# Performance work log

Measured on AMD Instinct MI355X. Metric: run time of the kernel, lower is better.

The kernel has to match this reference:

```python
import jax, jax.numpy as jnp
import numpy as np

B, NX, W, DX, DY, D, H, P = 8, 512, 16, 1536, 1024, 768, 12, 8


def setup_inputs() -> dict:
    key = jax.random.key(0)
    ks = jax.random.split(key, 12)
    r = lambda k, s: jax.random.normal(k, s, dtype=jnp.float32) * 0.02
    return {
        "x": jax.random.normal(ks[0], (B, NX, DX), jnp.float32),
        "y": jax.random.normal(ks[1], (B, NX * W, DY), jnp.float32),
        "Wx": r(ks[2], (DX, D)), "bx": jnp.zeros((D,), jnp.float32),
        "Wy": r(ks[3], (DY, D)), "by": jnp.zeros((D,), jnp.float32),
        "prompt": r(ks[4], (1, P, D)),
        "Wq": r(ks[5], (D, D)), "bq": jnp.zeros((D,), jnp.float32),
        "Wk": r(ks[6], (D, D)), "bk": jnp.zeros((D,), jnp.float32),
        "Wv": r(ks[7], (D, D)), "bv": jnp.zeros((D,), jnp.float32),
        "Wo": r(ks[8], (D, D)), "bo": jnp.zeros((D,), jnp.float32),
        "ln_g": jnp.ones((D,), jnp.float32), "ln_b": jnp.zeros((D,), jnp.float32),
    }


def _l2n(f, eps=1e-6):
    return f / (jnp.linalg.norm(f, axis=-1, keepdims=True) + eps)


def reference(x, y, Wx, bx, Wy, by, prompt, Wq, bq, Wk, bk, Wv, bv, Wo, bo, ln_g, ln_b):
    dh = D // H
    scale = 1.0 / jnp.sqrt(jnp.float32(dh))
    xp = _l2n(x @ Wx + bx)            # [B,NX,D]
    yp = _l2n(y @ Wy + by)            # [B,NX*W,D]
    # In the original, only normalized_output[:,0:1] is kept per window, and
    # per-query attention is independent, so only query index 0 contributes.
    q = ((xp[:, 0] @ Wq) + bq).reshape(B, H, dh) * scale   # [B,H,dh]
    yw = yp.reshape(B, NX, W, D)                            # 16-token windows
    k = ((yw @ Wk) + bk).reshape(B, NX, W, H, dh)
    v = ((yw @ Wv) + bv).reshape(B, NX, W, H, dh)
    s = jnp.einsum('bhd,bnwhd->bhnw', q, k)                # [B,H,NX,W]
    a = jax.nn.softmax(s, axis=-1)
    ctx = jnp.einsum('bhnw,bnwhd->bnhd', a, v).reshape(B, NX, D)
    o = ctx @ Wo + bo                                      # attn out_proj
    mu = jnp.mean(o, axis=-1, keepdims=True)
    var = jnp.var(o, axis=-1, keepdims=True)
    normed = (o - mu) / jnp.sqrt(var + 1e-6) * ln_g + ln_b  # [B,NX,D]
    blocks = jnp.concatenate(
        [normed[:, :, None, :],
         jnp.broadcast_to(prompt[:, None], (B, NX, P, D))], axis=2)  # [B,NX,1+P,D]
    return blocks.reshape(B, NX * (1 + P), D)
```

## Files before the change

kernel.cpp:

```cpp
#include <hip/hip_runtime.h>
#include <stdint.h>

#define BQ 8
#define NXQ 512
#define WQ 16
#define DXQ 1536
#define DYQ 1024
#define DQ 768
#define HQ 12
#define PQ 8
#define MY 65536
#define BN_ROWS 4096

typedef __attribute__((ext_vector_type(8))) short short8;
typedef __attribute__((ext_vector_type(4))) float f32x4;
typedef unsigned short ushort_t;
typedef unsigned int uint_t;

__device__ __forceinline__ ushort_t f2bf(float f) {
  uint_t u = __float_as_uint(f);
  u += 0x7FFFu + ((u >> 16) & 1u);
  return (ushort_t)(u >> 16);
}
__device__ __forceinline__ float bf2f(ushort_t h) {
  return __uint_as_float(((uint_t)h) << 16);
}
__device__ __forceinline__ void gload_lds16(const void* g, void* l) {
  __builtin_amdgcn_global_load_lds(
      (__attribute__((address_space(1))) unsigned int*)(g),
      (__attribute__((address_space(3))) unsigned int*)(l), 16, 0, 0);
}

__global__ void k_conv(const float* __restrict__ y, const float* __restrict__ Wy,
                       const float* __restrict__ Wv, const float* __restrict__ Wo,
                       ushort_t* __restrict__ ybf, ushort_t* __restrict__ WyT,
                       ushort_t* __restrict__ WvT, ushort_t* __restrict__ WoT,
                       float* __restrict__ rowsq, float* __restrict__ oS12,
                       float* __restrict__ xw) {
  const int gstride = gridDim.x * blockDim.x;
  const int g0 = blockIdx.x * blockDim.x + threadIdx.x;
  const int NY8 = MY * DYQ / 8;
  for (int i = g0; i < NY8; i += gstride) {
    const float4* s = (const float4*)(y + (size_t)i * 8);
    float4 f0 = s[0], f1 = s[1];
    short8 hv;
    hv[0] = (short)f2bf(f0.x); hv[1] = (short)f2bf(f0.y);
    hv[2] = (short)f2bf(f0.z); hv[3] = (short)f2bf(f0.w);
    hv[4] = (short)f2bf(f1.x); hv[5] = (short)f2bf(f1.y);
    hv[6] = (short)f2bf(f1.z); hv[7] = (short)f2bf(f1.w);
    *(short8*)(ybf + (size_t)i * 8) = hv;
  }
  for (int i = g0; i < MY; i += gstride) rowsq[i] = 0.f;
  for (int i = g0; i < 2 * BN_ROWS; i += gstride) oS12[i] = 0.f;
  for (int i = g0; i < BQ * DQ; i += gstride) xw[i] = 0.f;
  const int N1 = DQ * DYQ;
  const int N2 = DQ * DQ;
  const int total = N1 + 2 * N2;
  for (int i = g0; i < total; i += gstride) {
    if (i < N1) {
      int n = i / DYQ, k = i - n * DYQ;
      WyT[i] = f2bf(Wy[k * DQ + n]);
    } else if (i < N1 + N2) {
      int j = i - N1;
      int n = j / DQ, k = j - n * DQ;
      WvT[j] = f2bf(Wv[k * DQ + n]);
    } else {
      int j = i - N1 - N2;
      int n = j / DQ, k = j - n * DQ;
      WoT[j] = f2bf(Wo[k * DQ + n]);
    }
  }
}

__global__ __launch_bounds__(128) void k_q1(const float* __restrict__ x,
                                            const float* __restrict__ Wx,
                                            const float* __restrict__ bx,
                                            float* __restrict__ xw) {
  const int b = blockIdx.x, c = blockIdx.y * 128 + threadIdx.x;
  const int kc = blockIdx.z;
  const float* xr = x + (size_t)b * NXQ * DXQ + kc * 192;
  const float* wp = Wx + (size_t)kc * 192 * DQ + c;
  float acc = (kc == 0) ? bx[c] : 0.f;
  for (int k = 0; k < 192; ++k) acc += xr[k] * wp[(size_t)k * DQ];
  atomicAdd(&xw[b * DQ + c], acc);
}

__global__ __launch_bounds__(128) void k_q2(const float* __restrict__ xw,
                                            const float* __restrict__ Wq,
                                            const float* __restrict__ bq,
                                            float* __restrict__ qv) {
  const int b = blockIdx.x, c = blockIdx.y * 128 + threadIdx.x;
  const float* xr = xw + b * DQ;
  float acc = 0.f, ss = 0.f;
  for (int k = 0; k < DQ; ++k) {
    float v = xr[k];
    acc += v * Wq[(size_t)k * DQ + c];
    ss += v * v;
  }
  const float inv = 1.0f / (sqrtf(ss) + 1e-6f);
  qv[b * DQ + c] = (acc * inv + bq[c]) * 0.125f;
}

__global__ void k_q3(const float* __restrict__ Wk, const float* __restrict__ bk,
                     const float* __restrict__ qv, float* __restrict__ qk,
                     float* __restrict__ cQ) {
  const int bh = blockIdx.x;
  const int b = bh / HQ, h = bh - b * HQ;
  const int tid = threadIdx.x;
  const float* q = qv + b * DQ + h * 64;
#pragma unroll
  for (int j = 0; j < 3; ++j) {
    int dd = tid + j * 256;
    float acc = 0.f;
    for (int j2 = 0; j2 < 64; ++j2) acc += Wk[(size_t)dd * DQ + h * 64 + j2] * q[j2];
    qk[(size_t)bh * DQ + dd] = acc;
  }
  if (tid == 0) {
    float acc = 0.f;
    for (int j2 = 0; j2 < 64; ++j2) acc += q[j2] * bk[h * 64 + j2];
    cQ[bh] = acc;
  }
}

__global__ __launch_bounds__(512, 1) void k_gemm_yp(const ushort_t* __restrict__ ybf,
                                                    const ushort_t* __restrict__ WyT,
                                                    const float* __restrict__ by,
                                                    ushort_t* __restrict__ z,
                                                    float* __restrict__ rowsqg) {
  __shared__ __align__(16) char smem[131072 + 1024];
  float* rowsq_l = (float*)(smem + 131072);
  const int tid = threadIdx.x, lane = tid & 63, wv = tid >> 6;
  const int wvM = wv >> 2, wvN = wv & 3;
  const int g = blockIdx.x;
  const int m = (g / 24) * 8 + (g & 7);
  const int n = (g >> 3) % 3;
  const int mBase = m * 256, nBase = n * 256;
  if (tid < 256) rowsq_l[tid] = 0.f;

  const int sr = lane >> 2;
  const int sc = (lane & 3) ^ (sr & 3);
  const ushort_t* aQ[2]; const ushort_t* bQ[2];
  int qDst[2];
#pragma unroll
  for (int j = 0; j < 2; ++j) {
    int r = wv * 32 + j * 16 + sr;
    aQ[j] = ybf + (size_t)(mBase + r) * DYQ + sc * 8;
    bQ[j] = WyT + (size_t)(nBase + r) * DYQ + sc * 8;
    qDst[j] = (wv * 32 + j * 16) * 64;
  }
  const int q = lane >> 4;
  int aFr[8], bFr[4];
#pragma unroll
  for (int mf = 0; mf < 8; ++mf) {
    int r = wvM * 128 + mf * 16 + (lane & 15);
    aFr[mf] = r * 64 + ((q ^ (r & 3)) << 4);
  }
#pragma unroll
  for (int nf = 0; nf < 4; ++nf) {
    int r = wvN * 64 + nf * 16 + (lane & 15);
    bFr[nf] = 16384 + r * 64 + ((q ^ (r & 3)) << 4);
  }

#define YP_STAGE(pp)                                                           \
  {                                                                            \
    char* db = smem + ((pp) & 3) * 32768;                                      \
    const int koff = ((pp) >> 1) * 64 + ((pp) & 1) * 32;                       \
    _Pragma("unroll") for (int j = 0; j < 2; ++j)                              \
        gload_lds16(aQ[j] + koff, db + qDst[j]);                               \
    _Pragma("unroll") for (int j = 0; j < 2; ++j)                              \
        gload_lds16(bQ[j] + koff, db + 16384 + qDst[j]);                       \
  }

  f32x4 acc[8][4] = {};
  YP_STAGE(0);
  YP_STAGE(1);
  YP_STAGE(2);
  asm volatile("s_waitcnt vmcnt(8)" ::: "memory");
  __builtin_amdgcn_s_barrier();
  __builtin_amdgcn_sched_barrier(0);

  for (int t = 0; t < 16; ++t) {
#pragma unroll
    for (int ks = 0; ks < 2; ++ks) {
      const int p = 2 * t + ks;
      const char* cb = smem + (p & 3) * 32768;
      short8 af[8], bf[4];
#pragma unroll
      for (int mf = 0; mf < 8; ++mf) af[mf] = *(const short8*)(cb + aFr[mf]);
#pragma unroll
      for (int nf = 0; nf < 4; ++nf) bf[nf] = *(const short8*)(cb + bFr[nf]);
      if (p <= 28) YP_STAGE(p + 3);
      asm volatile("s_waitcnt lgkmcnt(0)" ::: "memory");
      __builtin_amdgcn_sched_barrier(0);
      __builtin_amdgcn_s_setprio(1);
#pragma unroll
      for (int nf = 0; nf < 4; ++nf)
#pragma unroll
        for (int mf = 0; mf < 8; ++mf)
          acc[mf][nf] = __builtin_amdgcn_mfma_f32_16x16x32_bf16(af[mf], bf[nf],
                                                                acc[mf][nf], 0, 0, 0);
      __builtin_amdgcn_s_setprio(0);
      __builtin_amdgcn_sched_barrier(0);
      if (p <= 28) {
        asm volatile("s_waitcnt vmcnt(8)" ::: "memory");
      } else if (p == 29) {
        asm volatile("s_waitcnt vmcnt(4)" ::: "memory");
      } else {
        asm volatile("s_waitcnt vmcnt(0)" ::: "memory");
      }
      __builtin_amdgcn_s_barrier();
      __builtin_amdgcn_sched_barrier(0);
    }
  }
  __syncthreads();

  float byv[4];
#pragma unroll
  for (int nf = 0; nf < 4; ++nf) byv[nf] = by[nBase + wvN * 64 + nf * 16 + (lane & 15)];
#pragma unroll
  for (int mf = 0; mf < 8; ++mf) {
#pragma unroll
    for (int rr = 0; rr < 4; ++rr) {
      int row_l = wvM * 128 + mf * 16 + (lane >> 4) * 4 + rr;
      float ss = 0.f;
#pragma unroll
      for (int nf = 0; nf < 4; ++nf) {
        float zv = acc[mf][nf][rr] + byv[nf];
        ss += zv * zv;
        int col_l = wvN * 64 + nf * 16 + (lane & 15);
        *(ushort_t*)(smem + row_l * 512 + col_l * 2) = f2bf(zv);
      }
#pragma unroll
      for (int o = 1; o < 16; o <<= 1) ss += __shfl_xor(ss, o, 64);
      if ((lane & 15) == 0) atomicAdd(&rowsq_l[row_l], ss);
    }
  }
  __syncthreads();
  if (tid < 256) atomicAdd(&rowsqg[mBase + tid], rowsq_l[tid]);
#pragma unroll
  for (int it = 0; it < 16; ++it) {
    int row = it * 16 + (tid >> 5);
    int ch = tid & 31;
    uint4 v = *(const uint4*)(smem + row * 512 + ch * 16);
    *(uint4*)(z + (size_t)(mBase + row) * DQ + nBase + ch * 8) = v;
  }
}

__global__ __launch_bounds__(256) void k_attn(const ushort_t* __restrict__ z,
                                              const float* __restrict__ rowsqg,
                                              const float* __restrict__ qk,
                                              const float* __restrict__ cQ,
                                              ushort_t* __restrict__ p) {
  __shared__ __align__(16) char smem[16 * 1552 + 192 * 4 * 2 + 64];
  float* s_l = (float*)(smem + 16 * 1552);
  float* a_l = s_l + 192;
  float* inv_l = a_l + 192;
  const int bn = blockIdx.x, b = bn >> 9;
  const int tid = threadIdx.x;
  if (tid < 16) inv_l[tid] = 1.0f / (sqrtf(rowsqg[bn * 16 + tid]) + 1e-6f);
  for (int j = tid; j < 16 * 96; j += 256) {
    int w = j / 96, ch = j - w * 96;
    *(short8*)(smem + w * 1552 + ch * 16) =
        *(const short8*)(z + ((size_t)bn * 16 + w) * DQ + ch * 8);
  }
  __syncthreads();
  if (tid < 192) {
    int h = tid >> 4, w = tid & 15;
    const float4* qkp = (const float4*)(qk + (size_t)(b * HQ + h) * DQ);
    float acc = 0.f;
    const char* yrow = smem + w * 1552;
    for (int dc = 0; dc < 192; ++dc) {
      float4 q4 = qkp[dc];
      uint2 hh = *(const uint2*)(yrow + dc * 8);
      acc += q4.x * bf2f((ushort_t)(hh.x & 0xffff));
      acc += q4.y * bf2f((ushort_t)(hh.x >> 16));
      acc += q4.z * bf2f((ushort_t)(hh.y & 0xffff));
      acc += q4.w * bf2f((ushort_t)(hh.y >> 16));
    }
    s_l[tid] = acc * inv_l[w] + cQ[b * HQ + h];
  }
  __syncthreads();
  if (tid < 12) {
    float mx = -1e30f;
#pragma unroll
    for (int w = 0; w < 16; ++w) mx = fmaxf(mx, s_l[tid * 16 + w]);
    float sm = 0.f, ev[16];
#pragma unroll
    for (int w = 0; w < 16; ++w) {
      ev[w] = __expf(s_l[tid * 16 + w] - mx);
      sm += ev[w];
    }
    float rden = 1.0f / sm;
#pragma unroll
    for (int w = 0; w < 16; ++w) a_l[tid * 16 + w] = ev[w] * rden * inv_l[w];
  }
  __syncthreads();
  float zr[16][3];
#pragma unroll
  for (int w = 0; w < 16; ++w)
#pragma unroll
    for (int i = 0; i < 3; ++i)
      zr[w][i] = bf2f(*(const ushort_t*)(smem + w * 1552 + (tid + i * 256) * 2));
  for (int h = 0; h < HQ; ++h) {
    float acc0 = 0.f, acc1 = 0.f, acc2 = 0.f;
#pragma unroll
    for (int w = 0; w < 16; ++w) {
      float aw = a_l[h * 16 + w];
      acc0 += aw * zr[w][0];
      acc1 += aw * zr[w][1];
      acc2 += aw * zr[w][2];
    }
    size_t base = ((size_t)bn * HQ + h) * DQ + tid;
    p[base] = f2bf(acc0);
    p[base + 256] = f2bf(acc1);
    p[base + 512] = f2bf(acc2);
  }
}

#define PV_TSZ 24576
__global__ __launch_bounds__(256) void k_gemm_pv(const ushort_t* __restrict__ p,
                                                 const ushort_t* __restrict__ WvT,
                                                 const float* __restrict__ bv,
                                                 ushort_t* __restrict__ ctx) {
  __shared__ __align__(16) char smem[3 * PV_TSZ];
  const int tid = threadIdx.x, lane = tid & 63, wv = tid >> 6;
  const int wvM = wv >> 1, wvN = wv & 1;
  const int mBase = blockIdx.x * 128, h = blockIdx.y;
  const int l8 = lane >> 3;
  const int c8 = (lane & 7) ^ (l8 & 7);
  const ushort_t* aSrc[4]; const ushort_t* bSrc[2];
  int aDst[4], bDst[2];
#pragma unroll
  for (int j = 0; j < 4; ++j) {
    int r = wv * 32 + j * 8 + l8;
    aSrc[j] = p + ((size_t)(mBase + r) * HQ + h) * DQ + c8 * 8;
    aDst[j] = (wv * 32 + j * 8) * 128;
  }
#pragma unroll
  for (int j = 0; j < 2; ++j) {
    int r = wv * 16 + j * 8 + l8;
    bSrc[j] = WvT + (size_t)(h * 64 + r) * DQ + c8 * 8;
    bDst[j] = 16384 + (wv * 16 + j * 8) * 128;
  }
  const int q = lane >> 4;
  int aRowB[4], aSw[4], bRowB[2], bSw[2];
#pragma unroll
  for (int mf = 0; mf < 4; ++mf) {
    int r = wvM * 64 + mf * 16 + (lane & 15);
    aRowB[mf] = r * 128; aSw[mf] = r & 7;
  }
#pragma unroll
  for (int nf = 0; nf < 2; ++nf) {
    int r = wvN * 32 + nf * 16 + (lane & 15);
    bRowB[nf] = 16384 + r * 128; bSw[nf] = r & 7;
  }
#define PV_STAGE(dbuf, t)                                                      \
  {                                                                            \
    char* db = smem + (dbuf) * PV_TSZ;                                         \
    _Pragma("unroll") for (int j = 0; j < 4; ++j)                              \
        gload_lds16(aSrc[j] + (t) * 64, db + aDst[j]);                         \
    _Pragma("unroll") for (int j = 0; j < 2; ++j)                              \
        gload_lds16(bSrc[j] + (t) * 64, db + bDst[j]);                         \
  }
  f32x4 acc[4][2] = {};
  PV_STAGE(0, 0);
  PV_STAGE(1, 1);
  int bR = 0, bS = 2;
  for (int t = 0; t < 12; ++t) {
    if (t < 11) {
      asm volatile("s_waitcnt vmcnt(6)" ::: "memory");
    } else {
      asm volatile("s_waitcnt vmcnt(0)" ::: "memory");
    }
    __builtin_amdgcn_s_barrier();
    __builtin_amdgcn_sched_barrier(0);
    if (t + 2 < 12) PV_STAGE(bS, t + 2);
    const char* cur = smem + bR * PV_TSZ;
#pragma unroll
    for (int ks = 0; ks < 2; ++ks) {
      short8 af[4], bf[2];
#pragma unroll
      for (int mf = 0; mf < 4; ++mf)
        af[mf] = *(const short8*)(cur + aRowB[mf] + (((ks * 4 + q) ^ aSw[mf]) << 4));
#pragma unroll
      for (int nf = 0; nf < 2; ++nf)
        bf[nf] = *(const short8*)(cur + bRowB[nf] + (((ks * 4 + q) ^ bSw[nf]) << 4));
#pragma unroll
      for (int nf = 0; nf < 2; ++nf)
#pragma unroll
        for (int mf = 0; mf < 4; ++mf)
          acc[mf][nf] = __builtin_amdgcn_mfma_f32_16x16x32_bf16(af[mf], bf[nf],
                                                                acc[mf][nf], 0, 0, 0);
    }
    bR = (bR == 2) ? 0 : bR + 1;
    bS = (bS == 2) ? 0 : bS + 1;
  }
#pragma unroll
  for (int nf = 0; nf < 2; ++nf) {
    int col = h * 64 + wvN * 32 + nf * 16 + (lane & 15);
    float bvv = bv[col];
#pragma unroll
    for (int mf = 0; mf < 4; ++mf)
#pragma unroll
      for (int rr = 0; rr < 4; ++rr) {
        int row = mBase + wvM * 64 + mf * 16 + (lane >> 4) * 4 + rr;
        ctx[(size_t)row * DQ + col] = f2bf(acc[mf][nf][rr] + bvv);
      }
  }
}

__global__ __launch_bounds__(256) void k_gemm_o(const ushort_t* __restrict__ ctx,
                                                const ushort_t* __restrict__ WoT,
                                                const float* __restrict__ bo,
                                                float* __restrict__ o,
                                                float* __restrict__ oS12) {
  __shared__ __align__(16) char smem[3 * PV_TSZ];
  const int tid = threadIdx.x, lane = tid & 63, wv = tid >> 6;
  const int wvM = wv >> 1, wvN = wv & 1;
  const int mBase = blockIdx.x * 128, nBase = blockIdx.y * 64;
  const int l8 = lane >> 3;
  const int c8 = (lane & 7) ^ (l8 & 7);
  const ushort_t* aSrc[4]; const ushort_t* bSrc[2];
  int aDst[4], bDst[2];
#pragma unroll
  for (int j = 0; j < 4; ++j) {
    int r = wv * 32 + j * 8 + l8;
    aSrc[j] = ctx + (size_t)(mBase + r) * DQ + c8 * 8;
    aDst[j] = (wv * 32 + j * 8) * 128;
  }
#pragma unroll
  for (int j = 0; j < 2; ++j) {
    int r = wv * 16 + j * 8 + l8;
    bSrc[j] = WoT + (size_t)(nBase + r) * DQ + c8 * 8;
    bDst[j] = 16384 + (wv * 16 + j * 8) * 128;
  }
  const int q = lane >> 4;
  int aRowB[4], aSw[4], bRowB[2], bSw[2];
#pragma unroll
  for (int mf = 0; mf < 4; ++mf) {
    int r = wvM * 64 + mf * 16 + (lane & 15);
    aRowB[mf] = r * 128; aSw[mf] = r & 7;
  }
#pragma unroll
  for (int nf = 0; nf < 2; ++nf) {
    int r = wvN * 32 + nf * 16 + (lane & 15);
    bRowB[nf] = 16384 + r * 128; bSw[nf] = r & 7;
  }
  f32x4 acc[4][2] = {};
#define O_STAGE(dbuf, t)                                                       \
  {                                                                            \
    char* db = smem + (dbuf) * PV_TSZ;                                         \
    _Pragma("unroll") for (int j = 0; j < 4; ++j)                              \
        gload_lds16(aSrc[j] + (t) * 64, db + aDst[j]);                         \
    _Pragma("unroll") for (int j = 0; j < 2; ++j)                              \
        gload_lds16(bSrc[j] + (t) * 64, db + bDst[j]);                         \
  }
  O_STAGE(0, 0);
  O_STAGE(1, 1);
  int bR = 0, bS = 2;
  for (int t = 0; t < 12; ++t) {
    if (t < 11) {
      asm volatile("s_waitcnt vmcnt(6)" ::: "memory");
    } else {
      asm volatile("s_waitcnt vmcnt(0)" ::: "memory");
    }
    __builtin_amdgcn_s_barrier();
    __builtin_amdgcn_sched_barrier(0);
    if (t + 2 < 12) O_STAGE(bS, t + 2);
    const char* cur = smem + bR * PV_TSZ;
#pragma unroll
    for (int ks = 0; ks < 2; ++ks) {
      short8 af[4], bf[2];
#pragma unroll
      for (int mf = 0; mf < 4; ++mf)
        af[mf] = *(const short8*)(cur + aRowB[mf] + (((ks * 4 + q) ^ aSw[mf]) << 4));
#pragma unroll
      for (int nf = 0; nf < 2; ++nf)
        bf[nf] = *(const short8*)(cur + bRowB[nf] + (((ks * 4 + q) ^ bSw[nf]) << 4));
#pragma unroll
      for (int nf = 0; nf < 2; ++nf)
#pragma unroll
        for (int mf = 0; mf < 4; ++mf)
          acc[mf][nf] = __builtin_amdgcn_mfma_f32_16x16x32_bf16(af[mf], bf[nf],
                                                                acc[mf][nf], 0, 0, 0);
    }
    bR = (bR == 2) ? 0 : bR + 1;
    bS = (bS == 2) ? 0 : bS + 1;
  }
  float bo0 = bo[nBase + wvN * 32 + (lane & 15)];
  float bo1 = bo[nBase + wvN * 32 + 16 + (lane & 15)];
#pragma unroll
  for (int mf = 0; mf < 4; ++mf)
#pragma unroll
    for (int rr = 0; rr < 4; ++rr) {
      int row = mBase + wvM * 64 + mf * 16 + (lane >> 4) * 4 + rr;
      float z0 = acc[mf][0][rr] + bo0;
      float z1 = acc[mf][1][rr] + bo1;
      o[(size_t)row * DQ + nBase + wvN * 32 + (lane & 15)] = z0;
      o[(size_t)row * DQ + nBase + wvN * 32 + 16 + (lane & 15)] = z1;
      float s1 = z0 + z1, s2 = z0 * z0 + z1 * z1;
#pragma unroll
      for (int ofs = 1; ofs < 16; ofs <<= 1) {
        s1 += __shfl_xor(s1, ofs, 64);
        s2 += __shfl_xor(s2, ofs, 64);
      }
      if ((lane & 15) == 0) {
        atomicAdd(&oS12[row], s1);
        atomicAdd(&oS12[BN_ROWS + row], s2);
      }
    }
}

__global__ __launch_bounds__(256) void k_out(const float* __restrict__ o,
                                             const float* __restrict__ oS12,
                                             const float* __restrict__ ln_g,
                                             const float* __restrict__ ln_b,
                                             const float* __restrict__ prompt,
                                             float* __restrict__ out) {
  const int row = blockIdx.x;
  const int tid = threadIdx.x;
  float mu = oS12[row] * (1.0f / DQ);
  float va = oS12[BN_ROWS + row] * (1.0f / DQ) - mu * mu;
  float rstd = rsqrtf(va + 1e-6f);
  int b = row >> 9, n = row & 511;
  size_t obase = ((size_t)b * (NXQ * (PQ + 1)) + (size_t)n * (PQ + 1)) * DQ;
#pragma unroll
  for (int j = 0; j < 3; ++j) {
    int col = tid + j * 256;
    out[obase + col] = (o[(size_t)row * DQ + col] - mu) * rstd * ln_g[col] + ln_b[col];
  }
#pragma unroll
  for (int pi = 0; pi < PQ; ++pi)
#pragma unroll
    for (int j = 0; j < 3; ++j) {
      int col = tid + j * 256;
      out[obase + (size_t)(1 + pi) * DQ + col] = prompt[pi * DQ + col];
    }
}

extern "C" void kernel_launch(void* const* d_in, const int* in_sizes, int n_in,
                              void* d_out, int out_size, void* d_ws, size_t ws_size,
                              hipStream_t stream) {
  (void)in_sizes; (void)n_in; (void)out_size; (void)ws_size;
  const float* x    = (const float*)d_in[0];
  const float* y    = (const float*)d_in[1];
  const float* Wx   = (const float*)d_in[2];
  const float* bx   = (const float*)d_in[3];
  const float* Wy   = (const float*)d_in[4];
  const float* by   = (const float*)d_in[5];
  const float* prom = (const float*)d_in[6];
  const float* Wq   = (const float*)d_in[7];
  const float* bq   = (const float*)d_in[8];
  const float* Wk   = (const float*)d_in[9];
  const float* bk   = (const float*)d_in[10];
  const float* Wv   = (const float*)d_in[11];
  const float* bv   = (const float*)d_in[12];
  const float* Wo   = (const float*)d_in[13];
  const float* bo   = (const float*)d_in[14];
  const float* lng  = (const float*)d_in[15];
  const float* lnb  = (const float*)d_in[16];
  float* out = (float*)d_out;
  char* ws = (char*)d_ws;

  size_t oWyT = 0;
  size_t oWvT = oWyT + (size_t)DQ * DYQ * 2;
  size_t oWoT = oWvT + (size_t)DQ * DQ * 2;
  size_t oXw  = oWoT + (size_t)DQ * DQ * 2;
  size_t oQ   = oXw + (size_t)BQ * DQ * 4 + 256;
  size_t oQK  = oQ + (size_t)BQ * DQ * 4;
  size_t oC   = oQK + (size_t)BQ * HQ * DQ * 4;
  size_t oRq  = oC + 1024;
  size_t oS   = oRq + (size_t)MY * 4;
  size_t oYbf = oS + (size_t)2 * BN_ROWS * 4;
  size_t oZ   = oYbf + (size_t)MY * DYQ * 2;
  size_t oP   = oYbf;
  size_t oCtx = oYbf + (size_t)BN_ROWS * HQ * DQ * 2;
  size_t oO   = oZ;

  ushort_t* WyT = (ushort_t*)(ws + oWyT);
  ushort_t* WvT = (ushort_t*)(ws + oWvT);
  ushort_t* WoT = (ushort_t*)(ws + oWoT);
  float* xw  = (float*)(ws + oXw);
  float* qv  = (float*)(ws + oQ);
  float* qk  = (float*)(ws + oQK);
  float* cQ  = (float*)(ws + oC);
  float* rowsq = (float*)(ws + oRq);
  float* oS12  = (float*)(ws + oS);
  ushort_t* ybf  = (ushort_t*)(ws + oYbf);
  ushort_t* zbuf = (ushort_t*)(ws + oZ);
  ushort_t* p    = (ushort_t*)(ws + oP);
  ushort_t* ctx  = (ushort_t*)(ws + oCtx);
  float* obuf    = (float*)(ws + oO);

  k_conv<<<dim3(4096), dim3(256), 0, stream>>>(y, Wy, Wv, Wo, ybf, WyT, WvT, WoT,
                                               rowsq, oS12, xw);
  k_q1<<<dim3(BQ, 6, 8), dim3(128), 0, stream>>>(x, Wx, bx, xw);
  k_q2<<<dim3(BQ, 6), dim3(128), 0, stream>>>(xw, Wq, bq, qv);
  k_q3<<<dim3(BQ * HQ), dim3(256), 0, stream>>>(Wk, bk, qv, qk, cQ);
  k_gemm_yp<<<dim3(768), dim3(512), 0, stream>>>(ybf, WyT, by, zbuf, rowsq);
  k_attn<<<dim3(BN_ROWS), dim3(256), 0, stream>>>(zbuf, rowsq, qk, cQ, p);
  k_gemm_pv<<<dim3(BN_ROWS / 128, HQ), dim3(256), 0, stream>>>(p, WvT, bv, ctx);
  k_gemm_o<<<dim3(BN_ROWS / 128, DQ / 64), dim3(256), 0, stream>>>(ctx, WoT, bo, obuf, oS12);
  k_out<<<dim3(BN_ROWS), dim3(256), 0, stream>>>(obuf, oS12, lng, lnb, prom, out);
}
```

Measured before the change: 446.9 us.

## Fold x-projection into conversion kernel and change LDS swizzle in yp GEMM

Removes the separate k_q1 launch and its atomics. The first 6144 threads of k_conv now compute the full-length x[:,0]@Wx dot product directly, so xw no longer needs zeroing. The yp GEMM's LDS XOR swizzle also changes from row-based to lane-bit-based, presumably to cut bank conflicts on fragment reads. The fused dot product runs 1536 serial iterations on a few blocks and may lengthen the conversion kernel's tail. The new swizzle must match between the store and load paths.

```diff
diff --git a/kernel.cpp b/kernel.cpp
--- a/kernel.cpp
+++ b/kernel.cpp
@@ -33,12 +33,21 @@
 
 __global__ void k_conv(const float* __restrict__ y, const float* __restrict__ Wy,
                        const float* __restrict__ Wv, const float* __restrict__ Wo,
+                       const float* __restrict__ x, const float* __restrict__ Wx,
+                       const float* __restrict__ bx,
                        ushort_t* __restrict__ ybf, ushort_t* __restrict__ WyT,
                        ushort_t* __restrict__ WvT, ushort_t* __restrict__ WoT,
                        float* __restrict__ rowsq, float* __restrict__ oS12,
                        float* __restrict__ xw) {
   const int gstride = gridDim.x * blockDim.x;
   const int g0 = blockIdx.x * blockDim.x + threadIdx.x;
+  if (g0 < BQ * DQ) {
+    int b = g0 / DQ, c = g0 - b * DQ;
+    const float* xr = x + (size_t)b * NXQ * DXQ;
+    float acc = bx[c];
+    for (int k = 0; k < DXQ; ++k) acc += xr[k] * Wx[(size_t)k * DQ + c];
+    xw[g0] = acc;
+  }
   const int NY8 = MY * DYQ / 8;
   for (int i = g0; i < NY8; i += gstride) {
     const float4* s = (const float4*)(y + (size_t)i * 8);
@@ -52,7 +61,6 @@
   }
   for (int i = g0; i < MY; i += gstride) rowsq[i] = 0.f;
   for (int i = g0; i < 2 * BN_ROWS; i += gstride) oS12[i] = 0.f;
-  for (int i = g0; i < BQ * DQ; i += gstride) xw[i] = 0.f;
   const int N1 = DQ * DYQ;
   const int N2 = DQ * DQ;
   const int total = N1 + 2 * N2;
@@ -72,19 +80,6 @@
   }
 }
 
-__global__ __launch_bounds__(128) void k_q1(const float* __restrict__ x,
-                                            const float* __restrict__ Wx,
-                                            const float* __restrict__ bx,
-                                            float* __restrict__ xw) {
-  const int b = blockIdx.x, c = blockIdx.y * 128 + threadIdx.x;
-  const int kc = blockIdx.z;
-  const float* xr = x + (size_t)b * NXQ * DXQ + kc * 192;
-  const float* wp = Wx + (size_t)kc * 192 * DQ + c;
-  float acc = (kc == 0) ? bx[c] : 0.f;
-  for (int k = 0; k < 192; ++k) acc += xr[k] * wp[(size_t)k * DQ];
-  atomicAdd(&xw[b * DQ + c], acc);
-}
-
 __global__ __launch_bounds__(128) void k_q2(const float* __restrict__ xw,
                                             const float* __restrict__ Wq,
                                             const float* __restrict__ bq,
@@ -138,7 +133,7 @@
   if (tid < 256) rowsq_l[tid] = 0.f;
 
   const int sr = lane >> 2;
-  const int sc = (lane & 3) ^ (sr & 3);
+  const int sc = (lane & 3) ^ ((lane >> 3) & 3);
   const ushort_t* aQ[2]; const ushort_t* bQ[2];
   int qDst[2];
 #pragma unroll
@@ -149,16 +144,17 @@
     qDst[j] = (wv * 32 + j * 16) * 64;
   }
   const int q = lane >> 4;
+  const int fsw = ((lane & 15) >> 1) & 3;
   int aFr[8], bFr[4];
 #pragma unroll
   for (int mf = 0; mf < 8; ++mf) {
     int r = wvM * 128 + mf * 16 + (lane & 15);
-    aFr[mf] = r * 64 + ((q ^ (r & 3)) << 4);
+    aFr[mf] = r * 64 + ((q ^ fsw) << 4);
   }
 #pragma unroll
   for (int nf = 0; nf < 4; ++nf) {
     int r = wvN * 64 + nf * 16 + (lane & 15);
-    bFr[nf] = 16384 + r * 64 + ((q ^ (r & 3)) << 4);
+    bFr[nf] = 16384 + r * 64 + ((q ^ fsw) << 4);
   }
 
 #define YP_STAGE(pp)                                                           \
@@ -592,9 +588,8 @@
   ushort_t* ctx  = (ushort_t*)(ws + oCtx);
   float* obuf    = (float*)(ws + oO);
 
-  k_conv<<<dim3(4096), dim3(256), 0, stream>>>(y, Wy, Wv, Wo, ybf, WyT, WvT, WoT,
-                                               rowsq, oS12, xw);
-  k_q1<<<dim3(BQ, 6, 8), dim3(128), 0, stream>>>(x, Wx, bx, xw);
+  k_conv<<<dim3(4096), dim3(256), 0, stream>>>(y, Wy, Wv, Wo, x, Wx, bx,
+                                               ybf, WyT, WvT, WoT, rowsq, oS12, xw);
   k_q2<<<dim3(BQ, 6), dim3(128), 0, stream>>>(xw, Wq, bq, qv);
   k_q3<<<dim3(BQ * HQ), dim3(256), 0, stream>>>(Wk, bk, qv, qk, cQ);
   k_gemm_yp<<<dim3(768), dim3(512), 0, stream>>>(ybf, WyT, by, zbuf, rowsq);
```

Result: slower. 532.8 us (+19.2%).
